# Kernel optimization log

Measured on AMD Instinct MI355X. Metric: run time of the kernel, lower is better.

Reference implementation:

```python
import jax, jax.numpy as jnp
import numpy as np

ITERS = 3; S = 8; I = 64; E = 64; C = 64; DIN = 128; SLOT = 128; H = 256
B = 64; N = 4096; EPS = 1e-8

def _ln(x, g, b):
    m = jnp.mean(x, -1, keepdims=True)
    v = jnp.var(x, -1, keepdims=True)
    return (x - m) * jax.lax.rsqrt(v + 1e-5) * g + b

def _gru(x, h, Wih, Whh, bih, bhh):
    # torch nn.GRUCell math; W stored as [in, 3*hidden]
    gi = x @ Wih + bih
    gh = h @ Whh + bhh
    ir, iz, inn = jnp.split(gi, 3, -1)
    hr, hz, hn = jnp.split(gh, 3, -1)
    r = jax.nn.sigmoid(ir + hr)
    z = jax.nn.sigmoid(iz + hz)
    n = jnp.tanh(inn + r * hn)
    return (1.0 - z) * n + z * h

def setup_inputs() -> dict:
    k = jax.random.split(jax.random.key(0), 32)
    d = {}
    d['slots_bck'] = jax.random.normal(k[0], (B, 1, SLOT), jnp.float32)
    d['inputs'] = jax.random.normal(k[1], (B, N, DIN), jnp.float32)
    d['protos'] = jax.random.normal(k[2], (C, I), jnp.float32)
    d['ext_noise'] = jax.random.normal(k[3], (B, S, E), jnp.float32)
    d['int_noise'] = jax.random.normal(k[4], (B, S, C), jnp.float32)
    u = jax.random.uniform(k[5], (ITERS, B, S, C), jnp.float32, 1e-6, 1.0 - 1e-6)
    d['gumbel'] = -jnp.log(-jnp.log(u))
    d['tau'] = 1
    w = lambda i, shape, s=0.05: jax.random.normal(k[i], shape, jnp.float32) * s
    d['ext_mu'] = w(6, (1, 1, E)); d['ext_log_sigma'] = w(7, (1, 1, E))
    d['int_mu'] = w(8, (1, 1, C)); d['int_log_sigma'] = w(9, (1, 1, C))
    d['ln_in_g'] = jnp.ones((DIN,)); d['ln_in_b'] = jnp.zeros((DIN,))
    d['ln_p_g'] = jnp.ones((I,)); d['ln_p_b'] = jnp.zeros((I,))
    d['ln_mi_g'] = jnp.ones((I,)); d['ln_mi_b'] = jnp.zeros((I,))
    d['ln_me_g'] = jnp.ones((E,)); d['ln_me_b'] = jnp.zeros((E,))
    d['Wq'] = w(10, (SLOT, SLOT)); d['Wk'] = w(11, (DIN, SLOT))
    d['Wv'] = w(12, (DIN, SLOT)); d['Wp'] = w(13, (I, I))
    d['gi_Wih'] = w(14, (I, 3 * I)); d['gi_Whh'] = w(15, (I, 3 * I))
    d['gi_bih'] = jnp.zeros((3 * I,)); d['gi_bhh'] = jnp.zeros((3 * I,))
    d['ge_Wih'] = w(16, (E, 3 * E)); d['ge_Whh'] = w(17, (E, 3 * E))
    d['ge_bih'] = jnp.zeros((3 * E,)); d['ge_bhh'] = jnp.zeros((3 * E,))
    d['mi_W1'] = w(18, (I, H)); d['mi_b1'] = jnp.zeros((H,))
    d['mi_W2'] = w(19, (H, I)); d['mi_b2'] = jnp.zeros((I,))
    d['me_W1'] = w(20, (E, H)); d['me_b1'] = jnp.zeros((H,))
    d['me_W2'] = w(21, (H, E)); d['me_b2'] = jnp.zeros((E,))
    return d

def reference(slots_bck, inputs, protos, ext_noise, int_noise, gumbel,
              ext_mu, ext_log_sigma, int_mu, int_log_sigma,
              ln_in_g, ln_in_b, ln_p_g, ln_p_b, ln_mi_g, ln_mi_b, ln_me_g, ln_me_b,
              Wq, Wk, Wv, Wp,
              gi_Wih, gi_Whh, gi_bih, gi_bhh, ge_Wih, ge_Whh, ge_bih, ge_bhh,
              mi_W1, mi_b1, mi_W2, mi_b2, me_W1, me_b1, me_W2, me_b2, tau):
    Bsz = inputs.shape[0]
    slots_ext = ext_mu + jnp.exp(ext_log_sigma) * ext_noise            # [B,S,E]
    logits_pi = int_mu + jnp.exp(int_log_sigma) * int_noise            # [B,S,C]
    x = _ln(inputs, ln_in_g, ln_in_b)
    kk = (x @ Wk) * (SLOT ** -0.5)                                     # [B,N,SLOT]
    vv = x @ Wv                                                        # [B,N,SLOT]
    p = _ln(protos, ln_p_g, ln_p_b) @ Wp                               # [C,I]
    attn_vis = None
    for i in range(ITERS):
        pi = jax.nn.softmax((logits_pi + gumbel[i]) / tau, axis=-1)    # soft gumbel-softmax
        slots_int = pi @ p                                             # [B,S,I]
        slots_obj = jnp.concatenate([slots_int, slots_ext], -1)        # [B,S,SLOT]
        slots = jnp.concatenate([slots_bck, slots_obj[:, 1:]], 1)
        q = slots @ Wq                                                 # [B,S,SLOT]
        attn_logits = jnp.einsum('bnd,bsd->bns', kk, q)
        attn_vis = jax.nn.softmax(attn_logits, -1)                     # softmax over slots
        attn = attn_vis + EPS
        attn = attn / jnp.sum(attn, -2, keepdims=True)                 # renorm over inputs
        updates = jnp.einsum('bns,bnd->bsd', attn, vv)                 # [B,S,SLOT]
        upd_int, upd_ext = updates[..., :I], updates[..., I:]
        slots_ext = _gru(upd_ext.reshape(-1, E), slots_ext.reshape(-1, E),
                         ge_Wih, ge_Whh, ge_bih, ge_bhh).reshape(Bsz, S, E)
        if i < ITERS - 1:
            h = _ln(slots_ext, ln_me_g, ln_me_b)
            slots_ext = slots_ext + (jax.nn.relu(h @ me_W1 + me_b1) @ me_W2 + me_b2)
        int_upd = _gru(upd_int.reshape(-1, I), slots_int.reshape(-1, I),
                       gi_Wih, gi_Whh, gi_bih, gi_bhh).reshape(Bsz, S, I)
        if i < ITERS - 1:
            h = _ln(int_upd, ln_mi_g, ln_mi_b)
            int_upd = int_upd + (jax.nn.relu(h @ mi_W1 + mi_b1) @ mi_W2 + mi_b2)
        logits_pi = (int_upd @ p.T) * (I ** -0.5)
    return slots_ext[:, 1:], logits_pi[:, 1:], attn_vis
```

## Files before the change

### kernel.cpp

```cpp
#include <hip/hip_runtime.h>
#include <hip/hip_bf16.h>
#include <stdint.h>

typedef unsigned short u16;
#define DEVFN static __device__ __forceinline__

typedef __attribute__((ext_vector_type(8))) short bf16x8;
typedef __attribute__((ext_vector_type(4))) float f32x4;

constexpr int   kB   = 64;
constexpr int   kN   = 4096;
constexpr float kEPS = 1e-8f;
constexpr float kLNE = 1e-5f;
constexpr float kKSC = 0.08838834764831845f;
constexpr float kISC = 0.125f;

DEVFN u16 f2bf(float f) {
    union { float f; uint32_t u; } x; x.f = f;
    uint32_t r = (x.u + 0x7fffu + ((x.u >> 16) & 1u)) >> 16;
    return (u16)r;
}
DEVFN uint32_t pk2(float lo, float hi) {
    __hip_bfloat162 h = __float22bfloat162_rn(make_float2(lo, hi));
    uint32_t u; __builtin_memcpy(&u, &h, 4); return u;
}
DEVFN u16 bf1(float f) {
    __hip_bfloat16 h = __float2bfloat16(f);
    u16 u; __builtin_memcpy(&u, &h, 2); return u;
}
DEVFN float sigf(float x) { return 1.0f / (1.0f + __expf(-x)); }
DEVFN float read_tau(const void* taup) {
    float inv_tau = 1.0f;
    int iv = *(const int*)taup;
    if (iv > 0 && iv < 1000000) inv_tau = 1.0f / (float)iv;
    else {
        float fv = *(const float*)taup;
        if (fv > 1e-6f && fv < 1e6f) inv_tau = 1.0f / fv;
    }
    return inv_tau;
}

__global__ void ksetup(const float* __restrict__ ext_mu, const float* __restrict__ ext_ls,
                       const float* __restrict__ int_mu, const float* __restrict__ int_ls,
                       const float* __restrict__ ext_noise, const float* __restrict__ int_noise,
                       float* __restrict__ sext, float* __restrict__ lpi,
                       const float* __restrict__ Wk, const float* __restrict__ Wv,
                       u16* __restrict__ WT,
                       const float* __restrict__ protos, const float* __restrict__ Wp,
                       const float* __restrict__ lpg, const float* __restrict__ lpb,
                       float* __restrict__ p, float* __restrict__ pT)
{
    __shared__ float pl[64][65];
    __shared__ float mS[64], sS[64];
    const int blk = blockIdx.x;
    const int t = threadIdx.x;
    if (blk < 128) {
        int idx = blk * 256 + t;
        int e = idx & 63;
        sext[idx] = ext_mu[e] + __expf(ext_ls[e]) * ext_noise[idx];
        lpi[idx]  = int_mu[e] + __expf(int_ls[e]) * int_noise[idx];
        return;
    }
    if (blk < 256) {
        int idx = (blk - 128) * 256 + t;
        int k = idx >> 8, c = idx & 255;
        float v = (c < 128) ? Wk[k * 128 + c] * kKSC : Wv[k * 128 + (c - 128)];
        WT[(size_t)c * 128 + k] = f2bf(v);
        return;
    }
    for (int idx = t; idx < 64 * 64; idx += 256) pl[idx >> 6][idx & 63] = protos[idx];
    __syncthreads();
    if (t < 64) {
        float sm = 0.f, sq = 0.f;
        for (int k = 0; k < 64; ++k) { float v = pl[t][k]; sm += v; sq += v * v; }
        float m = sm * (1.0f / 64.0f);
        float var = sq * (1.0f / 64.0f) - m * m;
        mS[t] = m; sS[t] = rsqrtf(var + kLNE);
    }
    __syncthreads();
    for (int idx = t; idx < 64 * 64; idx += 256) {
        int r = idx >> 6, c = idx & 63;
        pl[r][c] = (pl[r][c] - mS[r]) * sS[r] * lpg[c] + lpb[c];
    }
    __syncthreads();
    for (int idx = t; idx < 64 * 64; idx += 256) {
        int r = idx >> 6, c = idx & 63;
        float acc = 0.f;
        for (int k = 0; k < 64; ++k) acc += pl[r][k] * Wp[k * 64 + c];
        p[r * 64 + c] = acc;
        pT[c * 64 + r] = acc;
    }
}

__global__ void kslots(const float* __restrict__ lpi, const float* __restrict__ gum,
                       const void* __restrict__ taup,
                       const float* __restrict__ p,
                       const float* __restrict__ sbck, const float* __restrict__ sext,
                       const float* __restrict__ Wq,
                       float* __restrict__ sint, float* __restrict__ q)
{
    __shared__ float piL[64];
    __shared__ float sv[128];
    const int bs = blockIdx.x;
    const int t = threadIdx.x;
    const int b = bs >> 3, s = bs & 7;
    const float inv_tau = read_tau(taup);
    if (t < 64) {
        float l = (lpi[bs * 64 + t] + gum[bs * 64 + t]) * inv_tau;
        float m = l;
        #pragma unroll
        for (int d = 32; d >= 1; d >>= 1) m = fmaxf(m, __shfl_xor(m, d));
        float e = __expf(l - m);
        float smv = e;
        #pragma unroll
        for (int d = 32; d >= 1; d >>= 1) smv += __shfl_xor(smv, d);
        piL[t] = e / smv;
    }
    __syncthreads();
    if (t < 64) {
        float acc = 0.f;
        for (int c = 0; c < 64; ++c) acc += piL[c] * p[c * 64 + t];
        sint[bs * 64 + t] = acc;
        if (s == 0) {
            sv[t]      = sbck[b * 128 + t];
            sv[64 + t] = sbck[b * 128 + 64 + t];
        } else {
            sv[t]      = acc;
            sv[64 + t] = sext[bs * 64 + t];
        }
    }
    __syncthreads();
    {
        float acc = 0.f;
        for (int k = 0; k < 128; ++k) acc += sv[k] * Wq[k * 128 + t];
        q[bs * 128 + t] = acc;
    }
}

__global__ __launch_bounds__(256) void kmain(const float* __restrict__ inputs,
                                             const u16* __restrict__ WT,
                                             const float* __restrict__ lng, const float* __restrict__ lnb,
                                             const float* __restrict__ q0,
                                             u16* __restrict__ kk, u16* __restrict__ vvT,
                                             float* __restrict__ vpart,
                                             float* __restrict__ pu, float* __restrict__ pcs)
{
    __shared__ u16 At[64 * 128];
    __shared__ u16 Bt[128 * 64];
    __shared__ u16 qbf[16 * 128];
    __shared__ u16 aB[2][16][40];
    __shared__ float pwU[2][8][132];
    __shared__ float csL[2][8];
    const int t = threadIdx.x;
    const int blk = blockIdx.x;
    const int b = blk >> 6;
    const int n0 = (blk & 63) * 64;
    const float* inp = inputs + ((size_t)(b * kN + n0)) * 128;

    {
        float4 v = ((const float4*)(q0 + (size_t)b * 1024))[t];
        uint2 pk;
        pk.x = pk2(v.x, v.y);
        pk.y = pk2(v.z, v.w);
        *(uint2*)&qbf[(t >> 5) * 128 + (t & 31) * 4] = pk;
        ((uint32_t*)qbf)[512 + t] = 0u;
        ((uint32_t*)qbf)[768 + t] = 0u;
    }

    f32x4 xv[8];
    #pragma unroll
    for (int j = 0; j < 8; ++j)
        xv[j] = __builtin_nontemporal_load(((const f32x4*)inp) + t + j * 256);

    float s[8], qq[8];
    #pragma unroll
    for (int j = 0; j < 8; ++j) {
        s[j]  = xv[j][0] + xv[j][1] + xv[j][2] + xv[j][3];
        qq[j] = xv[j][0] * xv[j][0] + xv[j][1] * xv[j][1] + xv[j][2] * xv[j][2] + xv[j][3] * xv[j][3];
    }
    #pragma unroll
    for (int d = 16; d >= 1; d >>= 1) {
        #pragma unroll
        for (int j = 0; j < 8; ++j) {
            s[j]  += __shfl_xor(s[j], d);
            qq[j] += __shfl_xor(qq[j], d);
        }
    }
    const int col4 = t & 31;
    const float4 g4 = ((const float4*)lng)[col4];
    const float4 b4 = ((const float4*)lnb)[col4];
    #pragma unroll
    for (int j = 0; j < 8; ++j) {
        const int row = (t >> 5) + 8 * j;
        const float m   = s[j] * (1.0f / 128.0f);
        const float var = qq[j] * (1.0f / 128.0f) - m * m;
        const float sc  = rsqrtf(var + kLNE);
        uint32_t p0 = pk2((xv[j][0] - m) * sc * g4.x + b4.x, (xv[j][1] - m) * sc * g4.y + b4.y);
        uint32_t p1 = pk2((xv[j][2] - m) * sc * g4.z + b4.z, (xv[j][3] - m) * sc * g4.w + b4.w);
        const int byteoff = row * 256 + (((col4 >> 1) ^ (row & 7)) << 4) + ((col4 & 1) << 3);
        *(uint2*)((char*)At + byteoff) = make_uint2(p0, p1);
    }
    __syncthreads();

    const int w  = t >> 6;
    const int l  = t & 63;
    const int lg = l >> 4;
    const int lr = l & 15;
    const bool iskk = (w < 2);

    f32x4 acc[4][4];
    #pragma unroll
    for (int i = 0; i < 4; ++i)
        #pragma unroll
        for (int j = 0; j < 4; ++j) acc[i][j] = (f32x4){0.f, 0.f, 0.f, 0.f};

    #pragma unroll
    for (int ks = 0; ks < 4; ++ks) {
        bf16x8 wf[4], xf[4];
        #pragma unroll
        for (int i = 0; i < 4; ++i)
            wf[i] = *(const bf16x8*)(WT + (size_t)(w * 64 + 16 * i + lr) * 128 + ks * 32 + lg * 8);
        #pragma unroll
        for (int i = 0; i < 4; ++i) {
            const int r2 = 16 * i + lr;
            const int chunk = (ks * 4 + lg) ^ (r2 & 7);
            xf[i] = *(const bf16x8*)((const char*)At + r2 * 256 + chunk * 16);
        }
        if (iskk) {
            #pragma unroll
            for (int i = 0; i < 4; ++i)
                #pragma unroll
                for (int j = 0; j < 4; ++j)
                    acc[i][j] = __builtin_amdgcn_mfma_f32_16x16x32_bf16(wf[i], xf[j], acc[i][j], 0, 0, 0);
        } else {
            #pragma unroll
            for (int i = 0; i < 4; ++i)
                #pragma unroll
                for (int j = 0; j < 4; ++j)
                    acc[i][j] = __builtin_amdgcn_mfma_f32_16x16x32_bf16(xf[i], wf[j], acc[i][j], 0, 0, 0);
        }
    }

    __syncthreads();

    if (iskk) {
        #pragma unroll
        for (int cm = 0; cm < 4; ++cm) {
            const int c0 = w * 64 + 16 * cm + lg * 4;
            #pragma unroll
            for (int nn = 0; nn < 4; ++nn) {
                const int row = 16 * nn + lr;
                uint2 pk;
                pk.x = pk2(acc[cm][nn][0], acc[cm][nn][1]);
                pk.y = pk2(acc[cm][nn][2], acc[cm][nn][3]);
                const int byteoff = row * 256 + ((((c0 * 2) >> 4) ^ (row & 7)) << 4) + ((c0 * 2) & 15);
                *(uint2*)((char*)At + byteoff) = pk;
            }
        }
    } else {
        #pragma unroll
        for (int ct = 0; ct < 4; ++ct) {
            const int d = (w - 2) * 64 + 16 * ct + lr;
            #pragma unroll
            for (int m = 0; m < 4; ++m) {
                const int nn0 = 16 * m + lg * 4;
                uint2 pk;
                pk.x = pk2(acc[m][ct][0], acc[m][ct][1]);
                pk.y = pk2(acc[m][ct][2], acc[m][ct][3]);
                const int byteoff = d * 128 + ((((nn0 * 2) >> 4) ^ (d & 7)) << 4) + ((nn0 * 2) & 15);
                *(uint2*)((char*)Bt + byteoff) = pk;
            }
            float sv = 0.f;
            #pragma unroll
            for (int m = 0; m < 4; ++m)
                #pragma unroll
                for (int r = 0; r < 4; ++r) sv += acc[m][ct][r];
            sv += __shfl_xor(sv, 16);
            sv += __shfl_xor(sv, 32);
            if (lg == 0) __builtin_nontemporal_store(sv, &vpart[(size_t)blk * 128 + d]);
        }
    }
    __syncthreads();

    {
        const size_t kkbase = ((size_t)(b * kN) + n0) * 128;
        #pragma unroll
        for (int j = 0; j < 4; ++j) {
            const int cid = t + j * 256;
            const int row = cid >> 4, ci = cid & 15;
            uint4 v = *(const uint4*)((const char*)At + row * 256 + ((ci ^ (row & 7)) << 4));
            *(uint4*)(kk + kkbase + row * 128 + ci * 8) = v;
        }
        const size_t vvbase = (size_t)b * 128 * (size_t)kN + n0;
        #pragma unroll
        for (int j = 0; j < 4; ++j) {
            const int cid = t + j * 256;
            const int d = cid >> 3, ci = cid & 7;
            uint4 v = *(const uint4*)((const char*)Bt + d * 128 + ((ci ^ (d & 7)) << 4));
            *(uint4*)(vvT + vvbase + (size_t)d * kN + ci * 8) = v;
        }
    }

    if (w < 2) {
        bf16x8 qf[4];
        #pragma unroll
        for (int ks = 0; ks < 4; ++ks)
            qf[ks] = *(const bf16x8*)&qbf[lr * 128 + ks * 32 + lg * 8];
        f32x4 apv[8];
        #pragma unroll
        for (int dt = 0; dt < 8; ++dt) apv[dt] = (f32x4){0.f, 0.f, 0.f, 0.f};
        float cs0 = 0.f, cs1 = 0.f, cs2 = 0.f, cs3 = 0.f;
        #pragma unroll
        for (int c2 = 0; c2 < 2; ++c2) {
            const int rbase = w * 32 + c2 * 16;
            f32x4 plg = (f32x4){0.f, 0.f, 0.f, 0.f};
            #pragma unroll
            for (int ks = 0; ks < 4; ++ks) {
                const int row = rbase + lr;
                const int chunk = (ks * 4 + lg) ^ (row & 7);
                bf16x8 bfr = *(const bf16x8*)((const char*)At + row * 256 + chunk * 16);
                plg = __builtin_amdgcn_mfma_f32_16x16x32_bf16(qf[ks], bfr, plg, 0, 0, 0);
            }
            float m = fmaxf(fmaxf(plg[0], plg[1]), fmaxf(plg[2], plg[3]));
            m = fmaxf(m, __shfl_xor(m, 16));
            float e0 = __expf(plg[0] - m), e1 = __expf(plg[1] - m);
            float e2 = __expf(plg[2] - m), e3 = __expf(plg[3] - m);
            float smv = e0 + e1 + e2 + e3;
            smv += __shfl_xor(smv, 16);
            const float inv = 1.0f / smv;
            const float a0 = e0 * inv, a1 = e1 * inv, a2 = e2 * inv, a3 = e3 * inv;
            if (lg < 2) {
                cs0 += a0; cs1 += a1; cs2 += a2; cs3 += a3;
                const int s0 = lg * 4, nn = c2 * 16 + lr;
                aB[w][s0 + 0][nn] = bf1(a0);
                aB[w][s0 + 1][nn] = bf1(a1);
                aB[w][s0 + 2][nn] = bf1(a2);
                aB[w][s0 + 3][nn] = bf1(a3);
            }
        }
        bf16x8 af = *(const bf16x8*)&aB[w][lr][lg * 8];
        #pragma unroll
        for (int dt = 0; dt < 8; ++dt) {
            const int d = 16 * dt + lr;
            const int nc = (4 * w + lg) ^ (d & 7);
            bf16x8 vfr = *(const bf16x8*)((const char*)Bt + d * 128 + nc * 16);
            apv[dt] = __builtin_amdgcn_mfma_f32_16x16x32_bf16(vfr, af, apv[dt], 0, 0, 0);
        }
        if (lr < 8) {
            #pragma unroll
            for (int dt = 0; dt < 8; ++dt)
                *(float4*)&pwU[w][lr][16 * dt + lg * 4] =
                    make_float4(apv[dt][0], apv[dt][1], apv[dt][2], apv[dt][3]);
        }
        #pragma unroll
        for (int d2 = 8; d2 >= 1; d2 >>= 1) {
            cs0 += __shfl_xor(cs0, d2); cs1 += __shfl_xor(cs1, d2);
            cs2 += __shfl_xor(cs2, d2); cs3 += __shfl_xor(cs3, d2);
        }
        if (lr == 0 && lg < 2) {
            csL[w][lg * 4 + 0] = cs0; csL[w][lg * 4 + 1] = cs1;
            csL[w][lg * 4 + 2] = cs2; csL[w][lg * 4 + 3] = cs3;
        }
    }
    __syncthreads();
    {
        const int s2 = t >> 5, dq = t & 31;
        float4 r0 = *(const float4*)&pwU[0][s2][dq * 4];
        float4 r1 = *(const float4*)&pwU[1][s2][dq * 4];
        *(float4*)(pu + (size_t)blk * 1024 + s2 * 128 + dq * 4) =
            make_float4(r0.x + r1.x, r0.y + r1.y, r0.z + r1.z, r0.w + r1.w);
    }
    if (t < 8) pcs[blk * 8 + t] = csL[0][t] + csL[1][t];
}

__global__ void kvvsum(const float* __restrict__ part, float* __restrict__ vvsum)
{
    int t = blockIdx.x * 256 + threadIdx.x;
    int b = t >> 7, c = t & 127;
    float s = 0.f;
    const float* pp = part + (size_t)b * 64 * 128 + c;
    for (int nb = 0; nb < 64; ++nb) s += pp[nb * 128];
    vvsum[t] = s;
}

__global__ __launch_bounds__(256) void kattn(const u16* __restrict__ kk, const u16* __restrict__ vvT,
                                             const float* __restrict__ q,
                                             float* __restrict__ attn_out,
                                             float* __restrict__ pu, float* __restrict__ pcs,
                                             const int wvis)
{
    __shared__ u16 qbf[16][128];
    __shared__ u16 aB[4][16][40];
    __shared__ float pwU[4][8][132];
    __shared__ float csL[4][8];
    const int t = threadIdx.x;
    const int blk = blockIdx.x;
    const int b = blk >> 4;
    const int nb = blk & 15;
    const int w = t >> 6, l = t & 63, lg = l >> 4, lr = l & 15;

    {
        float4 v = ((const float4*)(q + (size_t)b * 1024))[t];
        uint2 pk;
        pk.x = pk2(v.x, v.y);
        pk.y = pk2(v.z, v.w);
        *(uint2*)&qbf[t >> 5][(t & 31) * 4] = pk;
        ((uint32_t*)qbf)[512 + t] = 0u;
        ((uint32_t*)qbf)[768 + (t & 255)] = 0u;
    }
    __syncthreads();

    bf16x8 qf[4];
    #pragma unroll
    for (int ks = 0; ks < 4; ++ks) qf[ks] = *(const bf16x8*)&qbf[lr][ks * 32 + lg * 8];

    f32x4 apv[8];
    #pragma unroll
    for (int dt = 0; dt < 8; ++dt) apv[dt] = (f32x4){0.f, 0.f, 0.f, 0.f};
    float cs0 = 0.f, cs1 = 0.f, cs2 = 0.f, cs3 = 0.f;

    const size_t kkb = (size_t)(b * kN) * 128;
    const size_t vvb = (size_t)b * 128 * (size_t)kN;

    #pragma unroll
    for (int ch = 0; ch < 2; ++ch) {
        const int nbase = nb * 256 + w * 64 + ch * 32;
        #pragma unroll
        for (int c2 = 0; c2 < 2; ++c2) {
            const int n16 = nbase + 16 * c2;
            f32x4 pl = (f32x4){0.f, 0.f, 0.f, 0.f};
            #pragma unroll
            for (int ks = 0; ks < 4; ++ks) {
                bf16x8 bfr = *(const bf16x8*)(kk + kkb + (size_t)(n16 + lr) * 128 + ks * 32 + lg * 8);
                pl = __builtin_amdgcn_mfma_f32_16x16x32_bf16(qf[ks], bfr, pl, 0, 0, 0);
            }
            float m = fmaxf(fmaxf(pl[0], pl[1]), fmaxf(pl[2], pl[3]));
            m = fmaxf(m, __shfl_xor(m, 16));
            float e0 = __expf(pl[0] - m), e1 = __expf(pl[1] - m);
            float e2 = __expf(pl[2] - m), e3 = __expf(pl[3] - m);
            float smv = e0 + e1 + e2 + e3;
            smv += __shfl_xor(smv, 16);
            const float inv = 1.0f / smv;
            const float a0 = e0 * inv, a1 = e1 * inv, a2 = e2 * inv, a3 = e3 * inv;
            if (lg < 2) {
                cs0 += a0; cs1 += a1; cs2 += a2; cs3 += a3;
                if (wvis)
                    *(float4*)(attn_out + ((size_t)(b * kN) + n16 + lr) * 8 + lg * 4) =
                        make_float4(a0, a1, a2, a3);
                const int s0 = lg * 4, nn = 16 * c2 + lr;
                aB[w][s0 + 0][nn] = bf1(a0);
                aB[w][s0 + 1][nn] = bf1(a1);
                aB[w][s0 + 2][nn] = bf1(a2);
                aB[w][s0 + 3][nn] = bf1(a3);
            }
        }
        bf16x8 af = *(const bf16x8*)&aB[w][lr][lg * 8];
        #pragma unroll
        for (int dt = 0; dt < 8; ++dt) {
            bf16x8 vfr = *(const bf16x8*)(vvT + vvb + (size_t)(16 * dt + lr) * kN + nbase + lg * 8);
            apv[dt] = __builtin_amdgcn_mfma_f32_16x16x32_bf16(vfr, af, apv[dt], 0, 0, 0);
        }
    }

    if (lr < 8) {
        #pragma unroll
        for (int dt = 0; dt < 8; ++dt)
            *(float4*)&pwU[w][lr][16 * dt + lg * 4] =
                make_float4(apv[dt][0], apv[dt][1], apv[dt][2], apv[dt][3]);
    }
    #pragma unroll
    for (int d = 8; d >= 1; d >>= 1) {
        cs0 += __shfl_xor(cs0, d); cs1 += __shfl_xor(cs1, d);
        cs2 += __shfl_xor(cs2, d); cs3 += __shfl_xor(cs3, d);
    }
    if (lr == 0 && lg < 2) {
        csL[w][lg * 4 + 0] = cs0; csL[w][lg * 4 + 1] = cs1;
        csL[w][lg * 4 + 2] = cs2; csL[w][lg * 4 + 3] = cs3;
    }
    __syncthreads();
    {
        const int s = t >> 5, dq = t & 31;
        float4 r0 = *(const float4*)&pwU[0][s][dq * 4];
        float4 r1 = *(const float4*)&pwU[1][s][dq * 4];
        float4 r2 = *(const float4*)&pwU[2][s][dq * 4];
        float4 r3 = *(const float4*)&pwU[3][s][dq * 4];
        float4 o;
        o.x = r0.x + r1.x + r2.x + r3.x;
        o.y = r0.y + r1.y + r2.y + r3.y;
        o.z = r0.z + r1.z + r2.z + r3.z;
        o.w = r0.w + r1.w + r2.w + r3.w;
        *(float4*)(pu + (size_t)blk * 1024 + s * 128 + dq * 4) = o;
    }
    if (t < 8) pcs[blk * 8 + t] = csL[0][t] + csL[1][t] + csL[2][t] + csL[3][t];
}

__global__ __launch_bounds__(256) void kupdate(
    const float* __restrict__ pu, const float* __restrict__ pcs, const int nblk,
    const float* __restrict__ vvsum, float* __restrict__ sint,
    float* __restrict__ sext, float* __restrict__ lpi,
    const float* __restrict__ giWih, const float* __restrict__ giWhh,
    const float* __restrict__ gibih, const float* __restrict__ gibhh,
    const float* __restrict__ geWih, const float* __restrict__ geWhh,
    const float* __restrict__ gebih, const float* __restrict__ gebhh,
    const float* __restrict__ miW1, const float* __restrict__ mib1,
    const float* __restrict__ miW2, const float* __restrict__ mib2,
    const float* __restrict__ meW1, const float* __restrict__ meb1,
    const float* __restrict__ meW2, const float* __restrict__ meb2,
    const float* __restrict__ lmig, const float* __restrict__ lmib,
    const float* __restrict__ lmeg, const float* __restrict__ lmeb,
    const float* __restrict__ pT, float* __restrict__ out, const int last,
    const float* __restrict__ gumN, const void* __restrict__ taup,
    const float* __restrict__ p, const float* __restrict__ sbck,
    const float* __restrict__ Wq, float* __restrict__ q)
{
    __shared__ float uL[128], hA[64], hB[64];
    __shared__ float g1[192], g2[192];
    __shared__ float tmp[256];
    __shared__ float outE[64], outI[64];
    __shared__ float lgL[64];
    __shared__ float sv[128];
    const int bs = blockIdx.x;
    const int b = bs >> 3, s = bs & 7;
    const int t = threadIdx.x;

    if (t < 128) {
        float num = 0.f;
        for (int nb = 0; nb < nblk; ++nb) num += pu[((size_t)(b * nblk + nb)) * 1024 + s * 128 + t];
        float den = 4096.0f * kEPS;
        for (int nb = 0; nb < nblk; ++nb) den += pcs[(b * nblk + nb) * 8 + s];
        uL[t] = (num + kEPS * vvsum[b * 128 + t]) / den;
    } else if (t < 192) {
        hA[t - 128] = sext[bs * 64 + (t - 128)];
    } else {
        hB[t - 192] = sint[bs * 64 + (t - 192)];
    }
    __syncthreads();
    if (t < 192) {
        float a = gebih[t], bb = gebhh[t];
        for (int k = 0; k < 64; ++k) {
            a  = fmaf(uL[64 + k], geWih[k * 192 + t], a);
            bb = fmaf(hA[k],      geWhh[k * 192 + t], bb);
        }
        g1[t] = a; g2[t] = bb;
    }
    __syncthreads();
    if (t < 64) {
        float r = sigf(g1[t] + g2[t]);
        float z = sigf(g1[64 + t] + g2[64 + t]);
        float nn = tanhf(g1[128 + t] + r * g2[128 + t]);
        outE[t] = (1.0f - z) * nn + z * hA[t];
    }
    __syncthreads();
    if (t < 192) {
        float a = gibih[t], bb = gibhh[t];
        for (int k = 0; k < 64; ++k) {
            a  = fmaf(uL[k], giWih[k * 192 + t], a);
            bb = fmaf(hB[k], giWhh[k * 192 + t], bb);
        }
        g1[t] = a; g2[t] = bb;
    }
    __syncthreads();
    if (t < 64) {
        float r = sigf(g1[t] + g2[t]);
        float z = sigf(g1[64 + t] + g2[64 + t]);
        float nn = tanhf(g1[128 + t] + r * g2[128 + t]);
        outI[t] = (1.0f - z) * nn + z * hB[t];
    }
    __syncthreads();
    if (!last) {
        if (t < 64) {
            float v = outE[t];
            float sm = v, sq = v * v;
            #pragma unroll
            for (int d = 32; d >= 1; d >>= 1) { sm += __shfl_xor(sm, d); sq += __shfl_xor(sq, d); }
            float m = sm * (1.0f / 64.0f), var = sq * (1.0f / 64.0f) - m * m;
            g1[t] = (v - m) * rsqrtf(var + kLNE) * lmeg[t] + lmeb[t];
        }
        __syncthreads();
        {
            float a = meb1[t];
            for (int k = 0; k < 64; ++k) a = fmaf(g1[k], meW1[k * 256 + t], a);
            tmp[t] = fmaxf(a, 0.0f);
        }
        __syncthreads();
        if (t < 64) {
            float o = meb2[t];
            for (int j = 0; j < 256; ++j) o = fmaf(tmp[j], meW2[j * 64 + t], o);
            outE[t] += o;
        }
        __syncthreads();
        if (t < 64) {
            float v = outI[t];
            float sm = v, sq = v * v;
            #pragma unroll
            for (int d = 32; d >= 1; d >>= 1) { sm += __shfl_xor(sm, d); sq += __shfl_xor(sq, d); }
            float m = sm * (1.0f / 64.0f), var = sq * (1.0f / 64.0f) - m * m;
            g1[t] = (v - m) * rsqrtf(var + kLNE) * lmig[t] + lmib[t];
        }
        __syncthreads();
        {
            float a = mib1[t];
            for (int k = 0; k < 64; ++k) a = fmaf(g1[k], miW1[k * 256 + t], a);
            tmp[t] = fmaxf(a, 0.0f);
        }
        __syncthreads();
        if (t < 64) {
            float o = mib2[t];
            for (int j = 0; j < 256; ++j) o = fmaf(tmp[j], miW2[j * 64 + t], o);
            outI[t] += o;
        }
        __syncthreads();
    }
    if (t < 64) {
        float lg = 0.f;
        for (int k = 0; k < 64; ++k) lg = fmaf(outI[k], pT[k * 64 + t], lg);
        lg *= kISC;
        lgL[t] = lg;
        if (last) { if (s > 0) out[28672 + (b * 7 + (s - 1)) * 64 + t] = lg; }
    } else if (t < 128) {
        int c = t - 64;
        float v = outE[c];
        sext[bs * 64 + c] = v;
        if (last && s > 0) out[(b * 7 + (s - 1)) * 64 + c] = v;
    }
    if (last) return;

    __syncthreads();
    const float inv_tau = read_tau(taup);
    if (t < 64) {
        float l = (lgL[t] + gumN[bs * 64 + t]) * inv_tau;
        float m = l;
        #pragma unroll
        for (int d = 32; d >= 1; d >>= 1) m = fmaxf(m, __shfl_xor(m, d));
        float e = __expf(l - m);
        float smv = e;
        #pragma unroll
        for (int d = 32; d >= 1; d >>= 1) smv += __shfl_xor(smv, d);
        tmp[t] = e / smv;
    }
    __syncthreads();
    if (t < 64) {
        float acc = 0.f;
        for (int c = 0; c < 64; ++c) acc += tmp[c] * p[c * 64 + t];
        sint[bs * 64 + t] = acc;
        if (s == 0) {
            sv[t]      = sbck[b * 128 + t];
            sv[64 + t] = sbck[b * 128 + 64 + t];
        } else {
            sv[t]      = acc;
            sv[64 + t] = outE[t];
        }
    }
    __syncthreads();
    if (t < 128) {
        float acc = 0.f;
        for (int k = 0; k < 128; ++k) acc += sv[k] * Wq[k * 128 + t];
        q[bs * 128 + t] = acc;
    }
}

extern "C" void kernel_launch(void* const* d_in, const int* in_sizes, int n_in,
                              void* d_out, int out_size, void* d_ws, size_t ws_size,
                              hipStream_t stream)
{
    (void)in_sizes; (void)n_in; (void)out_size; (void)ws_size;
    const float* slots_bck = (const float*)d_in[0];
    const float* inputs    = (const float*)d_in[1];
    const float* protos    = (const float*)d_in[2];
    const float* ext_noise = (const float*)d_in[3];
    const float* int_noise = (const float*)d_in[4];
    const float* gumbel    = (const float*)d_in[5];
    const void*  taup      = d_in[6];
    const float* ext_mu    = (const float*)d_in[7];
    const float* ext_ls    = (const float*)d_in[8];
    const float* int_mu    = (const float*)d_in[9];
    const float* int_ls    = (const float*)d_in[10];
    const float* ln_in_g   = (const float*)d_in[11];
    const float* ln_in_b   = (const float*)d_in[12];
    const float* ln_p_g    = (const float*)d_in[13];
    const float* ln_p_b    = (const float*)d_in[14];
    const float* ln_mi_g   = (const float*)d_in[15];
    const float* ln_mi_b   = (const float*)d_in[16];
    const float* ln_me_g   = (const float*)d_in[17];
    const float* ln_me_b   = (const float*)d_in[18];
    const float* Wq        = (const float*)d_in[19];
    const float* Wk        = (const float*)d_in[20];
    const float* Wv        = (const float*)d_in[21];
    const float* Wp        = (const float*)d_in[22];
    const float* giWih     = (const float*)d_in[23];
    const float* giWhh     = (const float*)d_in[24];
    const float* gibih     = (const float*)d_in[25];
    const float* gibhh     = (const float*)d_in[26];
    const float* geWih     = (const float*)d_in[27];
    const float* geWhh     = (const float*)d_in[28];
    const float* gebih     = (const float*)d_in[29];
    const float* gebhh     = (const float*)d_in[30];
    const float* miW1      = (const float*)d_in[31];
    const float* mib1      = (const float*)d_in[32];
    const float* miW2      = (const float*)d_in[33];
    const float* mib2      = (const float*)d_in[34];
    const float* meW1      = (const float*)d_in[35];
    const float* meb1      = (const float*)d_in[36];
    const float* meW2      = (const float*)d_in[37];
    const float* meb2      = (const float*)d_in[38];
    float* out = (float*)d_out;

    char* ws = (char*)d_ws;
    size_t o = 0;
    auto alloc = [&](size_t bytes) { size_t r = o; o += (bytes + 255) & ~(size_t)255; return r; };
    u16*   kkp   = (u16*)  (ws + alloc((size_t)kB * kN * 128 * 2));
    u16*   vvTp  = (u16*)  (ws + alloc((size_t)kB * kN * 128 * 2));
    u16*   WT    = (u16*)  (ws + alloc(256 * 128 * 2));
    float* vpart = (float*)(ws + alloc((size_t)4096 * 128 * 4));
    float* vvsum = (float*)(ws + alloc(8192 * 4));
    float* pbuf  = (float*)(ws + alloc(4096 * 4));
    float* pT    = (float*)(ws + alloc(4096 * 4));
    float* sext  = (float*)(ws + alloc(32768 * 4));
    float* lpi   = (float*)(ws + alloc(32768 * 4));
    float* sint  = (float*)(ws + alloc(32768 * 4));
    float* q     = (float*)(ws + alloc(65536 * 4));
    float* pu    = (float*)(ws + alloc((size_t)4096 * 1024 * 4));
    float* pcs   = (float*)(ws + alloc(4096 * 8 * 4));

    ksetup<<<257, 256, 0, stream>>>(ext_mu, ext_ls, int_mu, int_ls, ext_noise, int_noise,
                                    sext, lpi, Wk, Wv, WT, protos, Wp, ln_p_g, ln_p_b, pbuf, pT);
    kslots<<<512, 128, 0, stream>>>(lpi, gumbel, taup, pbuf, slots_bck, sext, Wq, sint, q);
    kmain<<<4096, 256, 0, stream>>>(inputs, WT, ln_in_g, ln_in_b, q, kkp, vvTp, vpart, pu, pcs);
    kvvsum<<<32, 256, 0, stream>>>(vpart, vvsum);

    for (int i = 0; i < 3; ++i) {
        const int last = (i == 2);
        if (i > 0)
            kattn<<<1024, 256, 0, stream>>>(kkp, vvTp, q, out + 57344, pu, pcs, last ? 1 : 0);
        kupdate<<<512, 256, 0, stream>>>(pu, pcs, (i == 0) ? 64 : 16, vvsum, sint, sext, lpi,
                                         giWih, giWhh, gibih, gibhh,
                                         geWih, geWhh, gebih, gebhh,
                                         miW1, mib1, miW2, mib2,
                                         meW1, meb1, meW2, meb2,
                                         ln_mi_g, ln_mi_b, ln_me_g, ln_me_b,
                                         pT, out, last,
                                         gumbel + (size_t)(i + 1 < 3 ? i + 1 : 0) * 32768,
                                         taup, pbuf, slots_bck, Wq, q);
    }
}
```

Measured before the change: 280.6 us.

## Process two input tiles per kmain block with loads prefetched, parallelize MLP second layer

```diff
diff --git a/kernel.cpp b/kernel.cpp
--- a/kernel.cpp
+++ b/kernel.cpp
@@ -152,10 +152,17 @@
     __shared__ float pwU[2][8][132];
     __shared__ float csL[2][8];
     const int t = threadIdx.x;
-    const int blk = blockIdx.x;
-    const int b = blk >> 6;
-    const int n0 = (blk & 63) * 64;
-    const float* inp = inputs + ((size_t)(b * kN + n0)) * 128;
+    const int g0 = blockIdx.x * 2;
+    const int b = g0 >> 6;
+
+    const int w  = t >> 6;
+    const int l  = t & 63;
+    const int lg = l >> 4;
+    const int lr = l & 15;
+    const bool iskk = (w < 2);
+    const int col4 = t & 31;
+    const float4 g4 = ((const float4*)lng)[col4];
+    const float4 b4 = ((const float4*)lnb)[col4];
 
     {
         float4 v = ((const float4*)(q0 + (size_t)b * 1024))[t];
@@ -167,210 +174,213 @@
         ((uint32_t*)qbf)[768 + t] = 0u;
     }
 
-    f32x4 xv[8];
-    #pragma unroll
-    for (int j = 0; j < 8; ++j)
-        xv[j] = __builtin_nontemporal_load(((const f32x4*)inp) + t + j * 256);
-
-    float s[8], qq[8];
-    #pragma unroll
-    for (int j = 0; j < 8; ++j) {
-        s[j]  = xv[j][0] + xv[j][1] + xv[j][2] + xv[j][3];
-        qq[j] = xv[j][0] * xv[j][0] + xv[j][1] * xv[j][1] + xv[j][2] * xv[j][2] + xv[j][3] * xv[j][3];
-    }
-    #pragma unroll
-    for (int d = 16; d >= 1; d >>= 1) {
+    f32x4 xvA[8], xvB[8];
+    {
+        const float* inpA = inputs + ((size_t)(b * kN) + (size_t)(g0 & 63) * 64) * 128;
+        const float* inpB = inpA + 64 * 128;
+        #pragma unroll
+        for (int j = 0; j < 8; ++j)
+            xvA[j] = __builtin_nontemporal_load(((const f32x4*)inpA) + t + j * 256);
+        #pragma unroll
+        for (int j = 0; j < 8; ++j)
+            xvB[j] = __builtin_nontemporal_load(((const f32x4*)inpB) + t + j * 256);
+    }
+
+    auto tile = [&](f32x4 (&xv)[8], const int g) {
+        const int n0 = (g & 63) * 64;
+        float s[8], qq[8];
         #pragma unroll
         for (int j = 0; j < 8; ++j) {
-            s[j]  += __shfl_xor(s[j], d);
-            qq[j] += __shfl_xor(qq[j], d);
-        }
-    }
-    const int col4 = t & 31;
-    const float4 g4 = ((const float4*)lng)[col4];
-    const float4 b4 = ((const float4*)lnb)[col4];
-    #pragma unroll
-    for (int j = 0; j < 8; ++j) {
-        const int row = (t >> 5) + 8 * j;
-        const float m   = s[j] * (1.0f / 128.0f);
-        const float var = qq[j] * (1.0f / 128.0f) - m * m;
-        const float sc  = rsqrtf(var + kLNE);
-        uint32_t p0 = pk2((xv[j][0] - m) * sc * g4.x + b4.x, (xv[j][1] - m) * sc * g4.y + b4.y);
-        uint32_t p1 = pk2((xv[j][2] - m) * sc * g4.z + b4.z, (xv[j][3] - m) * sc * g4.w + b4.w);
-        const int byteoff = row * 256 + (((col4 >> 1) ^ (row & 7)) << 4) + ((col4 & 1) << 3);
-        *(uint2*)((char*)At + byteoff) = make_uint2(p0, p1);
-    }
-    __syncthreads();
-
-    const int w  = t >> 6;
-    const int l  = t & 63;
-    const int lg = l >> 4;
-    const int lr = l & 15;
-    const bool iskk = (w < 2);
-
-    f32x4 acc[4][4];
-    #pragma unroll
-    for (int i = 0; i < 4; ++i)
-        #pragma unroll
-        for (int j = 0; j < 4; ++j) acc[i][j] = (f32x4){0.f, 0.f, 0.f, 0.f};
-
-    #pragma unroll
-    for (int ks = 0; ks < 4; ++ks) {
-        bf16x8 wf[4], xf[4];
+            s[j]  = xv[j][0] + xv[j][1] + xv[j][2] + xv[j][3];
+            qq[j] = xv[j][0] * xv[j][0] + xv[j][1] * xv[j][1] + xv[j][2] * xv[j][2] + xv[j][3] * xv[j][3];
+        }
+        #pragma unroll
+        for (int d = 16; d >= 1; d >>= 1) {
+            #pragma unroll
+            for (int j = 0; j < 8; ++j) {
+                s[j]  += __shfl_xor(s[j], d);
+                qq[j] += __shfl_xor(qq[j], d);
+            }
+        }
+        #pragma unroll
+        for (int j = 0; j < 8; ++j) {
+            const int row = (t >> 5) + 8 * j;
+            const float m   = s[j] * (1.0f / 128.0f);
+            const float var = qq[j] * (1.0f / 128.0f) - m * m;
+            const float sc  = rsqrtf(var + kLNE);
+            uint32_t p0 = pk2((xv[j][0] - m) * sc * g4.x + b4.x, (xv[j][1] - m) * sc * g4.y + b4.y);
+            uint32_t p1 = pk2((xv[j][2] - m) * sc * g4.z + b4.z, (xv[j][3] - m) * sc * g4.w + b4.w);
+            const int byteoff = row * 256 + (((col4 >> 1) ^ (row & 7)) << 4) + ((col4 & 1) << 3);
+            *(uint2*)((char*)At + byteoff) = make_uint2(p0, p1);
+        }
+        __syncthreads();
+
+        f32x4 acc[4][4];
         #pragma unroll
         for (int i = 0; i < 4; ++i)
-            wf[i] = *(const bf16x8*)(WT + (size_t)(w * 64 + 16 * i + lr) * 128 + ks * 32 + lg * 8);
-        #pragma unroll
-        for (int i = 0; i < 4; ++i) {
-            const int r2 = 16 * i + lr;
-            const int chunk = (ks * 4 + lg) ^ (r2 & 7);
-            xf[i] = *(const bf16x8*)((const char*)At + r2 * 256 + chunk * 16);
-        }
+            #pragma unroll
+            for (int j = 0; j < 4; ++j) acc[i][j] = (f32x4){0.f, 0.f, 0.f, 0.f};
+        #pragma unroll
+        for (int ks = 0; ks < 4; ++ks) {
+            bf16x8 wf[4], xf[4];
+            #pragma unroll
+            for (int i = 0; i < 4; ++i)
+                wf[i] = *(const bf16x8*)(WT + (size_t)(w * 64 + 16 * i + lr) * 128 + ks * 32 + lg * 8);
+            #pragma unroll
+            for (int i = 0; i < 4; ++i) {
+                const int r2 = 16 * i + lr;
+                const int chunk = (ks * 4 + lg) ^ (r2 & 7);
+                xf[i] = *(const bf16x8*)((const char*)At + r2 * 256 + chunk * 16);
+            }
+            if (iskk) {
+                #pragma unroll
+                for (int i = 0; i < 4; ++i)
+                    #pragma unroll
+                    for (int j = 0; j < 4; ++j)
+                        acc[i][j] = __builtin_amdgcn_mfma_f32_16x16x32_bf16(wf[i], xf[j], acc[i][j], 0, 0, 0);
+            } else {
+                #pragma unroll
+                for (int i = 0; i < 4; ++i)
+                    #pragma unroll
+                    for (int j = 0; j < 4; ++j)
+                        acc[i][j] = __builtin_amdgcn_mfma_f32_16x16x32_bf16(xf[i], wf[j], acc[i][j], 0, 0, 0);
+            }
+        }
+        __syncthreads();
+
         if (iskk) {
             #pragma unroll
-            for (int i = 0; i < 4; ++i)
+            for (int cm = 0; cm < 4; ++cm) {
+                const int c0 = w * 64 + 16 * cm + lg * 4;
                 #pragma unroll
-                for (int j = 0; j < 4; ++j)
-                    acc[i][j] = __builtin_amdgcn_mfma_f32_16x16x32_bf16(wf[i], xf[j], acc[i][j], 0, 0, 0);
+                for (int nn = 0; nn < 4; ++nn) {
+                    const int row = 16 * nn + lr;
+                    uint2 pk;
+                    pk.x = pk2(acc[cm][nn][0], acc[cm][nn][1]);
+                    pk.y = pk2(acc[cm][nn][2], acc[cm][nn][3]);
+                    const int byteoff = row * 256 + ((((c0 * 2) >> 4) ^ (row & 7)) << 4) + ((c0 * 2) & 15);
+                    *(uint2*)((char*)At + byteoff) = pk;
+                }
+            }
         } else {
             #pragma unroll
-            for (int i = 0; i < 4; ++i)
+            for (int ct = 0; ct < 4; ++ct) {
+                const int d = (w - 2) * 64 + 16 * ct + lr;
                 #pragma unroll
-                for (int j = 0; j < 4; ++j)
-                    acc[i][j] = __builtin_amdgcn_mfma_f32_16x16x32_bf16(xf[i], wf[j], acc[i][j], 0, 0, 0);
-        }
-    }
-
-    __syncthreads();
-
-    if (iskk) {
-        #pragma unroll
-        for (int cm = 0; cm < 4; ++cm) {
-            const int c0 = w * 64 + 16 * cm + lg * 4;
-            #pragma unroll
-            for (int nn = 0; nn < 4; ++nn) {
-                const int row = 16 * nn + lr;
-                uint2 pk;
-                pk.x = pk2(acc[cm][nn][0], acc[cm][nn][1]);
-                pk.y = pk2(acc[cm][nn][2], acc[cm][nn][3]);
-                const int byteoff = row * 256 + ((((c0 * 2) >> 4) ^ (row & 7)) << 4) + ((c0 * 2) & 15);
-                *(uint2*)((char*)At + byteoff) = pk;
-            }
-        }
-    } else {
-        #pragma unroll
-        for (int ct = 0; ct < 4; ++ct) {
-            const int d = (w - 2) * 64 + 16 * ct + lr;
-            #pragma unroll
-            for (int m = 0; m < 4; ++m) {
-                const int nn0 = 16 * m + lg * 4;
-                uint2 pk;
-                pk.x = pk2(acc[m][ct][0], acc[m][ct][1]);
-                pk.y = pk2(acc[m][ct][2], acc[m][ct][3]);
-                const int byteoff = d * 128 + ((((nn0 * 2) >> 4) ^ (d & 7)) << 4) + ((nn0 * 2) & 15);
-                *(uint2*)((char*)Bt + byteoff) = pk;
-            }
-            float sv = 0.f;
-            #pragma unroll
-            for (int m = 0; m < 4; ++m)
+                for (int m = 0; m < 4; ++m) {
+                    const int nn0 = 16 * m + lg * 4;
+                    uint2 pk;
+                    pk.x = pk2(acc[m][ct][0], acc[m][ct][1]);
+                    pk.y = pk2(acc[m][ct][2], acc[m][ct][3]);
+                    const int byteoff = d * 128 + ((((nn0 * 2) >> 4) ^ (d & 7)) << 4) + ((nn0 * 2) & 15);
+                    *(uint2*)((char*)Bt + byteoff) = pk;
+                }
+                float sv = 0.f;
                 #pragma unroll
-                for (int r = 0; r < 4; ++r) sv += acc[m][ct][r];
-            sv += __shfl_xor(sv, 16);
-            sv += __shfl_xor(sv, 32);
-            if (lg == 0) __builtin_nontemporal_store(sv, &vpart[(size_t)blk * 128 + d]);
-        }
-    }
-    __syncthreads();
-
-    {
-        const size_t kkbase = ((size_t)(b * kN) + n0) * 128;
-        #pragma unroll
-        for (int j = 0; j < 4; ++j) {
-            const int cid = t + j * 256;
-            const int row = cid >> 4, ci = cid & 15;
-            uint4 v = *(const uint4*)((const char*)At + row * 256 + ((ci ^ (row & 7)) << 4));
-            *(uint4*)(kk + kkbase + row * 128 + ci * 8) = v;
-        }
-        const size_t vvbase = (size_t)b * 128 * (size_t)kN + n0;
-        #pragma unroll
-        for (int j = 0; j < 4; ++j) {
-            const int cid = t + j * 256;
-            const int d = cid >> 3, ci = cid & 7;
-            uint4 v = *(const uint4*)((const char*)Bt + d * 128 + ((ci ^ (d & 7)) << 4));
-            *(uint4*)(vvT + vvbase + (size_t)d * kN + ci * 8) = v;
-        }
-    }
-
-    if (w < 2) {
-        bf16x8 qf[4];
-        #pragma unroll
-        for (int ks = 0; ks < 4; ++ks)
-            qf[ks] = *(const bf16x8*)&qbf[lr * 128 + ks * 32 + lg * 8];
-        f32x4 apv[8];
-        #pragma unroll
-        for (int dt = 0; dt < 8; ++dt) apv[dt] = (f32x4){0.f, 0.f, 0.f, 0.f};
-        float cs0 = 0.f, cs1 = 0.f, cs2 = 0.f, cs3 = 0.f;
-        #pragma unroll
-        for (int c2 = 0; c2 < 2; ++c2) {
-            const int rbase = w * 32 + c2 * 16;
-            f32x4 plg = (f32x4){0.f, 0.f, 0.f, 0.f};
-            #pragma unroll
-            for (int ks = 0; ks < 4; ++ks) {
-                const int row = rbase + lr;
-                const int chunk = (ks * 4 + lg) ^ (row & 7);
-                bf16x8 bfr = *(const bf16x8*)((const char*)At + row * 256 + chunk * 16);
-                plg = __builtin_amdgcn_mfma_f32_16x16x32_bf16(qf[ks], bfr, plg, 0, 0, 0);
-            }
-            float m = fmaxf(fmaxf(plg[0], plg[1]), fmaxf(plg[2], plg[3]));
-            m = fmaxf(m, __shfl_xor(m, 16));
-            float e0 = __expf(plg[0] - m), e1 = __expf(plg[1] - m);
-            float e2 = __expf(plg[2] - m), e3 = __expf(plg[3] - m);
-            float smv = e0 + e1 + e2 + e3;
-            smv += __shfl_xor(smv, 16);
-            const float inv = 1.0f / smv;
-            const float a0 = e0 * inv, a1 = e1 * inv, a2 = e2 * inv, a3 = e3 * inv;
-            if (lg < 2) {
-                cs0 += a0; cs1 += a1; cs2 += a2; cs3 += a3;
-                const int s0 = lg * 4, nn = c2 * 16 + lr;
-                aB[w][s0 + 0][nn] = bf1(a0);
-                aB[w][s0 + 1][nn] = bf1(a1);
-                aB[w][s0 + 2][nn] = bf1(a2);
-                aB[w][s0 + 3][nn] = bf1(a3);
-            }
-        }
-        bf16x8 af = *(const bf16x8*)&aB[w][lr][lg * 8];
-        #pragma unroll
-        for (int dt = 0; dt < 8; ++dt) {
-            const int d = 16 * dt + lr;
-            const int nc = (4 * w + lg) ^ (d & 7);
-            bf16x8 vfr = *(const bf16x8*)((const char*)Bt + d * 128 + nc * 16);
-            apv[dt] = __builtin_amdgcn_mfma_f32_16x16x32_bf16(vfr, af, apv[dt], 0, 0, 0);
-        }
-        if (lr < 8) {
-            #pragma unroll
-            for (int dt = 0; dt < 8; ++dt)
-                *(float4*)&pwU[w][lr][16 * dt + lg * 4] =
-                    make_float4(apv[dt][0], apv[dt][1], apv[dt][2], apv[dt][3]);
-        }
-        #pragma unroll
-        for (int d2 = 8; d2 >= 1; d2 >>= 1) {
-            cs0 += __shfl_xor(cs0, d2); cs1 += __shfl_xor(cs1, d2);
-            cs2 += __shfl_xor(cs2, d2); cs3 += __shfl_xor(cs3, d2);
-        }
-        if (lr == 0 && lg < 2) {
-            csL[w][lg * 4 + 0] = cs0; csL[w][lg * 4 + 1] = cs1;
-            csL[w][lg * 4 + 2] = cs2; csL[w][lg * 4 + 3] = cs3;
-        }
-    }
-    __syncthreads();
-    {
-        const int s2 = t >> 5, dq = t & 31;
-        float4 r0 = *(const float4*)&pwU[0][s2][dq * 4];
-        float4 r1 = *(const float4*)&pwU[1][s2][dq * 4];
-        *(float4*)(pu + (size_t)blk * 1024 + s2 * 128 + dq * 4) =
-            make_float4(r0.x + r1.x, r0.y + r1.y, r0.z + r1.z, r0.w + r1.w);
-    }
-    if (t < 8) pcs[blk * 8 + t] = csL[0][t] + csL[1][t];
+                for (int m = 0; m < 4; ++m)
+                    #pragma unroll
+                    for (int r = 0; r < 4; ++r) sv += acc[m][ct][r];
+                sv += __shfl_xor(sv, 16);
+                sv += __shfl_xor(sv, 32);
+                if (lg == 0) __builtin_nontemporal_store(sv, &vpart[(size_t)g * 128 + d]);
+            }
+        }
+        __syncthreads();
+
+        {
+            const size_t kkbase = ((size_t)(b * kN) + n0) * 128;
+            #pragma unroll
+            for (int j = 0; j < 4; ++j) {
+                const int cid = t + j * 256;
+                const int row = cid >> 4, ci = cid & 15;
+                uint4 v = *(const uint4*)((const char*)At + row * 256 + ((ci ^ (row & 7)) << 4));
+                *(uint4*)(kk + kkbase + row * 128 + ci * 8) = v;
+            }
+            const size_t vvbase = (size_t)b * 128 * (size_t)kN + n0;
+            #pragma unroll
+            for (int j = 0; j < 4; ++j) {
+                const int cid = t + j * 256;
+                const int d = cid >> 3, ci = cid & 7;
+                uint4 v = *(const uint4*)((const char*)Bt + d * 128 + ((ci ^ (d & 7)) << 4));
+                *(uint4*)(vvT + vvbase + (size_t)d * kN + ci * 8) = v;
+            }
+        }
+
+        if (w < 2) {
+            bf16x8 qf[4];
+            #pragma unroll
+            for (int ks = 0; ks < 4; ++ks)
+                qf[ks] = *(const bf16x8*)&qbf[lr * 128 + ks * 32 + lg * 8];
+            f32x4 apv[8];
+            #pragma unroll
+            for (int dt = 0; dt < 8; ++dt) apv[dt] = (f32x4){0.f, 0.f, 0.f, 0.f};
+            float cs0 = 0.f, cs1 = 0.f, cs2 = 0.f, cs3 = 0.f;
+            #pragma unroll
+            for (int c2 = 0; c2 < 2; ++c2) {
+                const int rbase = w * 32 + c2 * 16;
+                f32x4 plg = (f32x4){0.f, 0.f, 0.f, 0.f};
+                #pragma unroll
+                for (int ks = 0; ks < 4; ++ks) {
+                    const int row = rbase + lr;
+                    const int chunk = (ks * 4 + lg) ^ (row & 7);
+                    bf16x8 bfr = *(const bf16x8*)((const char*)At + row * 256 + chunk * 16);
+                    plg = __builtin_amdgcn_mfma_f32_16x16x32_bf16(qf[ks], bfr, plg, 0, 0, 0);
+                }
+                float m = fmaxf(fmaxf(plg[0], plg[1]), fmaxf(plg[2], plg[3]));
+                m = fmaxf(m, __shfl_xor(m, 16));
+                float e0 = __expf(plg[0] - m), e1 = __expf(plg[1] - m);
+                float e2 = __expf(plg[2] - m), e3 = __expf(plg[3] - m);
+                float smv = e0 + e1 + e2 + e3;
+                smv += __shfl_xor(smv, 16);
+                const float inv = 1.0f / smv;
+                const float a0 = e0 * inv, a1 = e1 * inv, a2 = e2 * inv, a3 = e3 * inv;
+                if (lg < 2) {
+                    cs0 += a0; cs1 += a1; cs2 += a2; cs3 += a3;
+                    const int s0 = lg * 4, nn = c2 * 16 + lr;
+                    aB[w][s0 + 0][nn] = bf1(a0);
+                    aB[w][s0 + 1][nn] = bf1(a1);
+                    aB[w][s0 + 2][nn] = bf1(a2);
+                    aB[w][s0 + 3][nn] = bf1(a3);
+                }
+            }
+            bf16x8 af = *(const bf16x8*)&aB[w][lr][lg * 8];
+            #pragma unroll
+            for (int dt = 0; dt < 8; ++dt) {
+                const int d = 16 * dt + lr;
+                const int nc = (4 * w + lg) ^ (d & 7);
+                bf16x8 vfr = *(const bf16x8*)((const char*)Bt + d * 128 + nc * 16);
+                apv[dt] = __builtin_amdgcn_mfma_f32_16x16x32_bf16(vfr, af, apv[dt], 0, 0, 0);
+            }
+            if (lr < 8) {
+                #pragma unroll
+                for (int dt = 0; dt < 8; ++dt)
+                    *(float4*)&pwU[w][lr][16 * dt + lg * 4] =
+                        make_float4(apv[dt][0], apv[dt][1], apv[dt][2], apv[dt][3]);
+            }
+            #pragma unroll
+            for (int d2 = 8; d2 >= 1; d2 >>= 1) {
+                cs0 += __shfl_xor(cs0, d2); cs1 += __shfl_xor(cs1, d2);
+                cs2 += __shfl_xor(cs2, d2); cs3 += __shfl_xor(cs3, d2);
+            }
+            if (lr == 0 && lg < 2) {
+                csL[w][lg * 4 + 0] = cs0; csL[w][lg * 4 + 1] = cs1;
+                csL[w][lg * 4 + 2] = cs2; csL[w][lg * 4 + 3] = cs3;
+            }
+        }
+        __syncthreads();
+        {
+            const int s2 = t >> 5, dq = t & 31;
+            float4 r0 = *(const float4*)&pwU[0][s2][dq * 4];
+            float4 r1 = *(const float4*)&pwU[1][s2][dq * 4];
+            *(float4*)(pu + (size_t)g * 1024 + s2 * 128 + dq * 4) =
+                make_float4(r0.x + r1.x, r0.y + r1.y, r0.z + r1.z, r0.w + r1.w);
+        }
+        if (t < 8) pcs[g * 8 + t] = csL[0][t] + csL[1][t];
+        __syncthreads();
+    };
+
+    tile(xvA, g0);
+    tile(xvB, g0 + 1);
 }
 
 __global__ void kvvsum(const float* __restrict__ part, float* __restrict__ vvsum)
@@ -516,6 +526,7 @@
     __shared__ float uL[128], hA[64], hB[64];
     __shared__ float g1[192], g2[192];
     __shared__ float tmp[256];
+    __shared__ float red[256];
     __shared__ float outE[64], outI[64];
     __shared__ float lgL[64];
     __shared__ float sv[128];
@@ -583,11 +594,17 @@
             tmp[t] = fmaxf(a, 0.0f);
         }
         __syncthreads();
-        if (t < 64) {
-            float o = meb2[t];
-            for (int j = 0; j < 256; ++j) o = fmaf(tmp[j], meW2[j * 64 + t], o);
-            outE[t] += o;
-        }
+        {
+            const int c = t & 63, qq = t >> 6;
+            float o = 0.f;
+            for (int jj = 0; jj < 64; ++jj) {
+                const int j = qq * 64 + jj;
+                o = fmaf(tmp[j], meW2[j * 64 + c], o);
+            }
+            red[t] = o;
+        }
+        __syncthreads();
+        if (t < 64) outE[t] += meb2[t] + red[t] + red[64 + t] + red[128 + t] + red[192 + t];
         __syncthreads();
         if (t < 64) {
             float v = outI[t];
@@ -604,11 +621,17 @@
             tmp[t] = fmaxf(a, 0.0f);
         }
         __syncthreads();
-        if (t < 64) {
-            float o = mib2[t];
-            for (int j = 0; j < 256; ++j) o = fmaf(tmp[j], miW2[j * 64 + t], o);
-            outI[t] += o;
-        }
+        {
+            const int c = t & 63, qq = t >> 6;
+            float o = 0.f;
+            for (int jj = 0; jj < 64; ++jj) {
+                const int j = qq * 64 + jj;
+                o = fmaf(tmp[j], miW2[j * 64 + c], o);
+            }
+            red[t] = o;
+        }
+        __syncthreads();
+        if (t < 64) outI[t] += mib2[t] + red[t] + red[64 + t] + red[128 + t] + red[192 + t];
         __syncthreads();
     }
     if (t < 64) {
@@ -725,7 +748,7 @@
     ksetup<<<257, 256, 0, stream>>>(ext_mu, ext_ls, int_mu, int_ls, ext_noise, int_noise,
                                     sext, lpi, Wk, Wv, WT, protos, Wp, ln_p_g, ln_p_b, pbuf, pT);
     kslots<<<512, 128, 0, stream>>>(lpi, gumbel, taup, pbuf, slots_bck, sext, Wq, sint, q);
-    kmain<<<4096, 256, 0, stream>>>(inputs, WT, ln_in_g, ln_in_b, q, kkp, vvTp, vpart, pu, pcs);
+    kmain<<<2048, 256, 0, stream>>>(inputs, WT, ln_in_g, ln_in_b, q, kkp, vvTp, vpart, pu, pcs);
     kvvsum<<<32, 256, 0, stream>>>(vpart, vvsum);
 
     for (int i = 0; i < 3; ++i) {
```

After: 303.6 us. 8.2% more time.
